# Kernel tuning notes

Hardware: AMD Instinct MI355X
Metric: run time of the kernel (lower is better)

The kernel has to match this reference:

```python
import jax, jax.numpy as jnp
import numpy as np

B, L, D, DEPTH, FF, VOCAB = 2, 2048, 1024, 4, 4096, 32000

def setup_inputs():
    key = jax.random.key(0)
    ks = jax.random.split(key, 16)
    n = lambda k, s, sc: jax.random.normal(k, s, dtype=jnp.float32) * sc
    sw = 0.01 / float(np.sqrt(D))  # xavier_normal with gain 0.01 on square dims
    return dict(
        tokens=jax.random.randint(ks[0], (B, L), 0, VOCAB),
        emb=n(ks[1], (VOCAB, D), 0.02),
        Wz=n(ks[2], (DEPTH, D, D), sw), bz=jnp.zeros((DEPTH, D)),
        Wza=n(ks[3], (DEPTH, D, D), sw), bza=jnp.zeros((DEPTH, D)),
        Wy=n(ks[4], (DEPTH, D, D), sw), by=jnp.zeros((DEPTH, D)),
        Wya=n(ks[5], (DEPTH, D, D), sw), bya=jnp.zeros((DEPTH, D)),
        lc_re=n(ks[6], (DEPTH, D), 1.0), lc_im=n(ks[7], (DEPTH, D), 1.0),
        g_in=jnp.ones((DEPTH, D)), g_sc=jnp.ones((DEPTH, D)), g_ffn=jnp.ones((DEPTH, D)),
        Wf=n(ks[8], (DEPTH, D, FF), 0.02), bf=jnp.zeros((DEPTH, FF)),
        Wfa=n(ks[9], (DEPTH, D, FF), 0.02), bfa=jnp.zeros((DEPTH, FF)),
        Wfo=n(ks[10], (DEPTH, FF, D), 0.02), bfo=jnp.zeros((DEPTH, D)),
        ln_w=jnp.ones((D,)), ln_b=jnp.zeros((D,)),
        Wout=n(ks[11], (D, VOCAB), 0.02), bout=jnp.zeros((VOCAB,)),
    )

def _silu(x):
    return x * jax.nn.sigmoid(x)

def _rms(x, w, eps=1e-6):
    return x * jax.lax.rsqrt(jnp.mean(x * x, axis=-1, keepdims=True) + eps) * w

def reference(tokens, emb, Wz, bz, Wza, bza, Wy, by, Wya, bya, lc_re, lc_im,
              g_in, g_sc, g_ffn, Wf, bf, Wfa, bfa, Wfo, bfo, ln_w, ln_b, Wout, bout):
    Bq, Lq = tokens.shape
    # Embedding with max_norm=1: torch renorms accessed rows to norm <= 1
    e = emb[tokens]
    nrm = jnp.linalg.norm(e, axis=-1, keepdims=True)
    x = e * jnp.minimum(1.0, 1.0 / jnp.maximum(nrm, 1e-7))
    # Decaying phazor kernel (shared across layers; phazor_angle_scale is a fixed buffer)
    angle = jnp.power(0.001, jnp.linspace(0.0, 1.0, D))
    ln_ph = (1e-5 + 1j * angle).astype(jnp.complex64)      # [D]
    t = jnp.arange(Lq, dtype=jnp.float32)
    ph = jnp.exp(t[:, None] * ln_ph[None, :])              # [L, D] complex
    pf = jnp.fft.fft(ph, n=2 * Lq, axis=0)                 # [2L, D]
    decay = jnp.exp(ln_ph)                                 # [D]
    for i in range(DEPTH):
        # --- SConv sublayer (pre-RMSNorm + residual) ---
        xr = x
        xn = _rms(x, g_sc[i])
        z = (xn @ Wz[i] + bz[i]) * _silu(xn @ Wza[i] + bza[i])
        zf = jnp.fft.fft(z.astype(jnp.complex64), n=2 * Lq, axis=1)
        h = jnp.fft.ifft(zf * pf[None], axis=1)[:, :Lq]    # inner-chunk causal decaying conv
        lc = (lc_re[i] + 1j * lc_im[i]).astype(jnp.complex64)
        h = h + lc[None, None, :] * ph[None] * decay[None, None, :]  # cross-chunk state carry
        y = (_rms(h.real, g_in[i]) @ Wy[i] + by[i]) * _silu(xn @ Wya[i] + bya[i])
        x = xr + y
        # --- FFN SwiGLU sublayer (pre-RMSNorm + residual) ---
        xr = x
        xn = _rms(x, g_ffn[i])
        x = xr + ((xn @ Wf[i] + bf[i]) * _silu(xn @ Wfa[i] + bfa[i])) @ Wfo[i] + bfo[i]
    # Final LayerNorm + vocab projection
    mu = jnp.mean(x, axis=-1, keepdims=True)
    var = jnp.mean((x - mu) ** 2, axis=-1, keepdims=True)
    x = (x - mu) * jax.lax.rsqrt(var + 1e-5) * ln_w + ln_b
    return x @ Wout + bout
```

## Files before the change

### kernel.cpp

```cpp
#include <hip/hip_runtime.h>
#include <math.h>

typedef __attribute__((ext_vector_type(8))) short bf16x8;
typedef __attribute__((ext_vector_type(4))) float f32x4;

#define DEVI __device__ __forceinline__

DEVI short f2bf(float f) {
  unsigned u = __builtin_bit_cast(unsigned, f);
  return (short)((u + 0x7fffu + ((u >> 16) & 1u)) >> 16);
}
DEVI float bf2f(short s) {
  unsigned u = ((unsigned)(unsigned short)s) << 16;
  return __builtin_bit_cast(float, u);
}

DEVI float silu_f(float v) { return v / (1.0f + expf(-v)); }

DEVI void async16(const void* g, void* l) {
  __builtin_amdgcn_global_load_lds(
      (const __attribute__((address_space(1))) void*)g,
      (__attribute__((address_space(3))) void*)l, 16, 0, 0);
}

template <int N>
DEVI void waitvm() { asm volatile("s_waitcnt vmcnt(%0)" ::"i"(N) : "memory"); }
DEVI void barrier_mem() { asm volatile("s_barrier" ::: "memory"); }

template <int NROWT>
DEVI void tile_map(int* bx, int* by) {
  const int nwg = gridDim.x;
  const int lin = blockIdx.x;
  const int q = nwg >> 3;
  const int wgid = (lin & 7) * q + (lin >> 3);
  *by = wgid % NROWT;
  *bx = wgid / NROWT;
}


template <int MODE, int BM, int BN, int WM, int WN, int NBUF, bool NT>
__global__ __launch_bounds__(256, 2) void gemm_k(const short* __restrict__ A,
                                                 const short* __restrict__ BT,
                                                 const float* __restrict__ bias,
                                                 void* __restrict__ outp,
                                                 int N, int K) {
  constexpr int MF = WM / 16, NF = WN / 16;
  constexpr int NWN = BN / WN;
  constexpr int PBB = (BM + BN) * 64;
  constexpr int DEPTH = NBUF - 1;
  constexpr int L = (BM + BN) / 64;
  static_assert((BM / WM) * (BN / WN) == 4, "4 waves");
  __shared__ __align__(16) char lds[NBUF * PBB];
  int bx, by;
  tile_map<4096 / BM>(&bx, &by);
  const int row0 = by * BM, col0 = bx * BN;
  const int t = threadIdx.x, w = t >> 6, lane = t & 63;
  const int wr = w / NWN, wc = w % NWN;
  f32x4 acc[MF][NF] = {};

  const int srow = t >> 2;
  const int sslot = (t & 3) ^ ((t >> 3) & 3);
  const char* gA0 = (const char*)A + ((size_t)(row0 + srow) * K) * 2 + sslot * 16;
  const char* gB0 = (const char*)BT + ((size_t)(col0 + srow) * K) * 2 + sslot * 16;
  const size_t ccstep = (size_t)K * 128;
  const int wb = w << 10;
  const int lr = lane & 15, ks = lane >> 4;

  const int NIT = K >> 5;
  auto stage = [&](int buf, int it) {
    char* dst = lds + buf * PBB;
    const size_t io = (size_t)it * 64;
#pragma unroll
    for (int cc = 0; cc < BM / 64; ++cc)
      async16(gA0 + io + cc * ccstep, dst + cc * 4096 + wb);
#pragma unroll
    for (int cc = 0; cc < BN / 64; ++cc)
      async16(gB0 + io + cc * ccstep, dst + BM * 64 + cc * 4096 + wb);
  };

#pragma unroll
  for (int pit = 0; pit < DEPTH; ++pit) stage(pit, pit);

  for (int it = 0; it < NIT; ++it) {
    const int rem = NIT - it;
    if (rem >= DEPTH + 1) waitvm<L * (DEPTH - 1)>();
    else if (rem >= 2) waitvm<L>();
    else waitvm<0>();
    barrier_mem();
    if (it + DEPTH < NIT) stage((it + DEPTH) % NBUF, it + DEPTH);
    const char* base = lds + (it % NBUF) * PBB;
    bf16x8 af[MF], bfr[NF];
#pragma unroll
    for (int m = 0; m < MF; ++m) {
      const int r = wr * WM + m * 16 + lr;
      af[m] = *(const bf16x8*)(base + r * 64 + ((ks ^ ((r >> 1) & 3)) << 4));
    }
#pragma unroll
    for (int n = 0; n < NF; ++n) {
      const int r = wc * WN + n * 16 + lr;
      bfr[n] = *(const bf16x8*)(base + BM * 64 + r * 64 + ((ks ^ ((r >> 1) & 3)) << 4));
    }
#pragma unroll
    for (int m = 0; m < MF; ++m)
#pragma unroll
      for (int n = 0; n < NF; ++n)
        acc[m][n] = __builtin_amdgcn_mfma_f32_16x16x32_bf16(af[m], bfr[n], acc[m][n], 0, 0, 0);
    __builtin_amdgcn_sched_barrier(0);
  }

  const int orow = row0 + wr * WM + (ks << 2);
  const int ocol = col0 + wc * WN + lr;
#pragma unroll
  for (int m = 0; m < MF; ++m) {
#pragma unroll
    for (int n = 0; n < NF; ++n) {
      const int c = ocol + (n << 4);
      const float bv = bias[c];
#pragma unroll
      for (int i = 0; i < 4; ++i) {
        const int r = orow + (m << 4) + i;
        const size_t idx = (size_t)r * N + c;
        float v = acc[m][n][i] + bv;
        if (MODE == 0) {
          if (NT) __builtin_nontemporal_store(v, &((float*)outp)[idx]);
          else ((float*)outp)[idx] = v;
        } else {
          ((float*)outp)[idx] += v;
        }
      }
    }
  }
}

template <int MODE, int BM, int BN, int WM, int WN, int NBUF>
__global__ __launch_bounds__(256, 2) void gemm2_k(const short* __restrict__ A1,
                                                  const short* __restrict__ A2,
                                                  const short* __restrict__ BT1,
                                                  const short* __restrict__ BT2,
                                                  const float* __restrict__ bias1,
                                                  const float* __restrict__ bias2,
                                                  void* __restrict__ outp,
                                                  int N, int K) {
  constexpr bool DUALA = (MODE == 1);
  constexpr int MF = WM / 16, NF = WN / 16;
  constexpr int NWN = BN / WN;
  constexpr int ABYTES = BM * 64 * (DUALA ? 2 : 1);
  constexpr int PBB = ABYTES + 2 * BN * 64;
  constexpr int DEPTH = NBUF - 1;
  constexpr int L = ((DUALA ? 2 : 1) * BM + 2 * BN) / 64;
  static_assert((BM / WM) * (BN / WN) == 4, "4 waves");
  __shared__ __align__(16) char lds[NBUF * PBB];
  int bx, by;
  tile_map<4096 / BM>(&bx, &by);
  const int row0 = by * BM, col0 = bx * BN;
  const int t = threadIdx.x, w = t >> 6, lane = t & 63;
  const int wr = w / NWN, wc = w % NWN;
  f32x4 acc1[MF][NF] = {}, acc2[MF][NF] = {};

  const int srow = t >> 2;
  const int sslot = (t & 3) ^ ((t >> 3) & 3);
  const size_t arow = ((size_t)(row0 + srow) * K) * 2 + sslot * 16;
  const size_t brow = ((size_t)(col0 + srow) * K) * 2 + sslot * 16;
  const char* gA1 = (const char*)A1 + arow;
  const char* gA2 = (const char*)A2 + arow;
  const char* gB1 = (const char*)BT1 + brow;
  const char* gB2 = (const char*)BT2 + brow;
  const size_t ccstep = (size_t)K * 128;
  const int wb = w << 10;
  const int lr = lane & 15, ks = lane >> 4;

  const int NIT = K >> 5;
  auto stage = [&](int buf, int it) {
    char* dst = lds + buf * PBB;
    const size_t io = (size_t)it * 64;
#pragma unroll
    for (int cc = 0; cc < BM / 64; ++cc) {
      async16(gA1 + io + cc * ccstep, dst + cc * 4096 + wb);
      if constexpr (DUALA)
        async16(gA2 + io + cc * ccstep, dst + BM * 64 + cc * 4096 + wb);
    }
#pragma unroll
    for (int cc = 0; cc < BN / 64; ++cc) {
      async16(gB1 + io + cc * ccstep, dst + ABYTES + cc * 4096 + wb);
      async16(gB2 + io + cc * ccstep, dst + ABYTES + BN * 64 + cc * 4096 + wb);
    }
  };

#pragma unroll
  for (int pit = 0; pit < DEPTH; ++pit) stage(pit, pit);

  for (int it = 0; it < NIT; ++it) {
    const int rem = NIT - it;
    if (rem >= DEPTH + 1) waitvm<L * (DEPTH - 1)>();
    else if (rem >= 2) waitvm<L>();
    else waitvm<0>();
    barrier_mem();
    if (it + DEPTH < NIT) stage((it + DEPTH) % NBUF, it + DEPTH);
    const char* base = lds + (it % NBUF) * PBB;
    bf16x8 af1[MF], af2[MF], bf1[NF], bf2[NF];
#pragma unroll
    for (int m = 0; m < MF; ++m) {
      const int r = wr * WM + m * 16 + lr;
      const int off = r * 64 + ((ks ^ ((r >> 1) & 3)) << 4);
      af1[m] = *(const bf16x8*)(base + off);
      if constexpr (DUALA) af2[m] = *(const bf16x8*)(base + BM * 64 + off);
    }
#pragma unroll
    for (int n = 0; n < NF; ++n) {
      const int r = wc * WN + n * 16 + lr;
      const int off = r * 64 + ((ks ^ ((r >> 1) & 3)) << 4);
      bf1[n] = *(const bf16x8*)(base + ABYTES + off);
      bf2[n] = *(const bf16x8*)(base + ABYTES + BN * 64 + off);
    }
#pragma unroll
    for (int m = 0; m < MF; ++m)
#pragma unroll
      for (int n = 0; n < NF; ++n) {
        acc1[m][n] = __builtin_amdgcn_mfma_f32_16x16x32_bf16(af1[m], bf1[n], acc1[m][n], 0, 0, 0);
        acc2[m][n] = __builtin_amdgcn_mfma_f32_16x16x32_bf16(DUALA ? af2[m] : af1[m], bf2[n],
                                                             acc2[m][n], 0, 0, 0);
      }
    __builtin_amdgcn_sched_barrier(0);
  }

  const int orow = row0 + wr * WM + (ks << 2);
  const int ocol = col0 + wc * WN + lr;
#pragma unroll
  for (int m = 0; m < MF; ++m) {
#pragma unroll
    for (int n = 0; n < NF; ++n) {
      const int c = ocol + (n << 4);
      const float bv1 = bias1[c], bv2 = bias2[c];
#pragma unroll
      for (int i = 0; i < 4; ++i) {
        const int r = orow + (m << 4) + i;
        const size_t idx = (size_t)r * N + c;
        const float g = (acc1[m][n][i] + bv1) * silu_f(acc2[m][n][i] + bv2);
        if (MODE == 1) ((float*)outp)[idx] += g;
        else ((short*)outp)[idx] = f2bf(g);
      }
    }
  }
}

__global__ __launch_bounds__(256) void transp_k(const float* __restrict__ W,
                                                short* __restrict__ WT,
                                                int R, int C) {
  __shared__ float tile[32][33];
  const size_t moff = (size_t)blockIdx.z * R * C;
  const float* Wp = W + moff;
  short* Tp = WT + moff;
  const int c0 = blockIdx.x << 5, r0 = blockIdx.y << 5;
  const int tx = threadIdx.x, ty = threadIdx.y;
#pragma unroll
  for (int i = 0; i < 4; ++i)
    tile[ty + 8 * i][tx] = Wp[(size_t)(r0 + ty + 8 * i) * C + (c0 + tx)];
  __syncthreads();
#pragma unroll
  for (int i = 0; i < 4; ++i)
    Tp[(size_t)(c0 + ty + 8 * i) * R + (r0 + tx)] = f2bf(tile[tx][ty + 8 * i]);
}

__global__ __launch_bounds__(256) void embed_k(const int* __restrict__ tok,
                                               const float* __restrict__ emb,
                                               float* __restrict__ x) {
  const int row = blockIdx.x, t = threadIdx.x, w = t >> 6, lane = t & 63;
  const int token = tok[row];
  float4 v = ((const float4*)(emb + (size_t)token * 1024))[t];
  float ss = v.x * v.x + v.y * v.y + v.z * v.z + v.w * v.w;
#pragma unroll
  for (int off = 32; off; off >>= 1) ss += __shfl_xor(ss, off, 64);
  __shared__ float red[4];
  if (lane == 0) red[w] = ss;
  __syncthreads();
  const float nrm = sqrtf(red[0] + red[1] + red[2] + red[3]);
  const float sc = fminf(1.0f, 1.0f / fmaxf(nrm, 1e-7f));
  v.x *= sc; v.y *= sc; v.z *= sc; v.w *= sc;
  ((float4*)(x + (size_t)row * 1024))[t] = v;
}

template <int BF>
__global__ __launch_bounds__(256) void rms_k(const void* __restrict__ xin,
                                             const float* __restrict__ g,
                                             short* __restrict__ o) {
  const int row = blockIdx.x, t = threadIdx.x, w = t >> 6, lane = t & 63;
  float v0, v1, v2, v3;
  if (BF) {
    short4 s = ((const short4*)((const short*)xin + (size_t)row * 1024))[t];
    v0 = bf2f(s.x); v1 = bf2f(s.y); v2 = bf2f(s.z); v3 = bf2f(s.w);
  } else {
    float4 v = ((const float4*)((const float*)xin + (size_t)row * 1024))[t];
    v0 = v.x; v1 = v.y; v2 = v.z; v3 = v.w;
  }
  float ss = v0 * v0 + v1 * v1 + v2 * v2 + v3 * v3;
#pragma unroll
  for (int off = 32; off; off >>= 1) ss += __shfl_xor(ss, off, 64);
  __shared__ float red[4];
  if (lane == 0) red[w] = ss;
  __syncthreads();
  const float sc = rsqrtf((red[0] + red[1] + red[2] + red[3]) * (1.0f / 1024.0f) + 1e-6f);
  float4 gv = ((const float4*)g)[t];
  short4 ov = make_short4(f2bf(v0 * sc * gv.x), f2bf(v1 * sc * gv.y),
                          f2bf(v2 * sc * gv.z), f2bf(v3 * sc * gv.w));
  *(short4*)(o + (size_t)row * 1024 + 4 * t) = ov;
}

__global__ __launch_bounds__(256) void ln_k(const float* __restrict__ x,
                                            const float* __restrict__ lw,
                                            const float* __restrict__ lb,
                                            short* __restrict__ o) {
  const int row = blockIdx.x, t = threadIdx.x, w = t >> 6, lane = t & 63;
  float4 v = ((const float4*)(x + (size_t)row * 1024))[t];
  float s1 = v.x + v.y + v.z + v.w;
  float s2 = v.x * v.x + v.y * v.y + v.z * v.z + v.w * v.w;
#pragma unroll
  for (int off = 32; off; off >>= 1) {
    s1 += __shfl_xor(s1, off, 64);
    s2 += __shfl_xor(s2, off, 64);
  }
  __shared__ float red[8];
  if (lane == 0) { red[w] = s1; red[4 + w] = s2; }
  __syncthreads();
  const float mu = (red[0] + red[1] + red[2] + red[3]) * (1.0f / 1024.0f);
  const float ex2 = (red[4] + red[5] + red[6] + red[7]) * (1.0f / 1024.0f);
  const float rs = rsqrtf(ex2 - mu * mu + 1e-5f);
  float4 wv = ((const float4*)lw)[t];
  float4 bv = ((const float4*)lb)[t];
  short4 ov = make_short4(f2bf((v.x - mu) * rs * wv.x + bv.x),
                          f2bf((v.y - mu) * rs * wv.y + bv.y),
                          f2bf((v.z - mu) * rs * wv.z + bv.z),
                          f2bf((v.w - mu) * rs * wv.w + bv.w));
  *(short4*)(o + (size_t)row * 1024 + 4 * t) = ov;
}

DEVI void decay_of(int d, float* dr, float* di) {
  const float ang = powf(1e-3f, (float)d * (1.0f / 1023.0f));
  float sn, cs;
  sincosf(ang, &sn, &cs);
  const float mag = expf(1e-5f);
  *dr = mag * cs; *di = mag * sn;
}

__global__ __launch_bounds__(256) void s1_k(const short* __restrict__ z,
                                            float* __restrict__ Er, float* __restrict__ Ei) {
  const int d = (blockIdx.x << 8) + threadIdx.x;
  const int c = blockIdx.y, b = blockIdx.z;
  float dr, di;
  decay_of(d, &dr, &di);
  const short* zp = z + ((size_t)(b * 2048 + c * 64) << 10) + d;
  float sr = 0.0f, si = 0.0f;
  for (int k = 0; k < 64; ++k) {
    float zv = bf2f(zp[(size_t)k << 10]);
    float nr = dr * sr - di * si + zv;
    si = dr * si + di * sr;
    sr = nr;
  }
  const int idx = ((b << 5) + c) * 1024 + d;
  Er[idx] = sr; Ei[idx] = si;
}

__global__ __launch_bounds__(256) void s2_k(const float* __restrict__ Er,
                                            const float* __restrict__ Ei,
                                            float* __restrict__ Sr, float* __restrict__ Si) {
  const int gid = (blockIdx.x << 8) + threadIdx.x;
  const int b = gid >> 10, d = gid & 1023;
  float dr, di;
  decay_of(d, &dr, &di);
  float ar = dr, ai = di;
#pragma unroll
  for (int q = 0; q < 6; ++q) { float nr = ar * ar - ai * ai; ai = 2.0f * ar * ai; ar = nr; }
  float sr = 0.0f, si = 0.0f;
  for (int c = 0; c < 32; ++c) {
    const int idx = ((b << 5) + c) * 1024 + d;
    Sr[idx] = sr; Si[idx] = si;
    const float er = Er[idx], ei = Ei[idx];
    const float nr = ar * sr - ai * si + er;
    si = ar * si + ai * sr + ei;
    sr = nr;
  }
}

__global__ __launch_bounds__(256) void s3_k(const short* __restrict__ z,
                                            const float* __restrict__ Sr,
                                            const float* __restrict__ Si,
                                            const float* __restrict__ lcre,
                                            const float* __restrict__ lcim,
                                            short* __restrict__ h) {
  const int d = (blockIdx.x << 8) + threadIdx.x;
  const int c = blockIdx.y, b = blockIdx.z;
  float dr, di;
  decay_of(d, &dr, &di);
  float ar = dr, ai = di;
#pragma unroll
  for (int q = 0; q < 6; ++q) { float nr = ar * ar - ai * ai; ai = 2.0f * ar * ai; ar = nr; }
  float wr = 1.0f, wi = 0.0f, br = ar, bi = ai;
  int e = c;
  while (e) {
    if (e & 1) { float nr = wr * br - wi * bi; wi = wr * bi + wi * br; wr = nr; }
    float nb = br * br - bi * bi; bi = 2.0f * br * bi; br = nb;
    e >>= 1;
  }
  { float nr = wr * dr - wi * di; wi = wr * di + wi * dr; wr = nr; }
  const int idx = ((b << 5) + c) * 1024 + d;
  float sr = Sr[idx], si = Si[idx];
  const float lr_ = lcre[d], li_ = lcim[d];
  const size_t base = ((size_t)(b * 2048 + c * 64) << 10) + d;
  for (int k = 0; k < 64; ++k) {
    const float zv = bf2f(z[base + ((size_t)k << 10)]);
    const float nr = dr * sr - di * si + zv;
    si = dr * si + di * sr;
    sr = nr;
    h[base + ((size_t)k << 10)] = f2bf(sr + lr_ * wr - li_ * wi);
    const float nw = wr * dr - wi * di;
    wi = wr * di + wi * dr;
    wr = nw;
  }
}

extern "C" void kernel_launch(void* const* d_in, const int* in_sizes, int n_in,
                              void* d_out, int out_size, void* d_ws, size_t ws_size,
                              hipStream_t stream) {
  const int* tokens = (const int*)d_in[0];
  const float* emb = (const float*)d_in[1];
  const float* Wz = (const float*)d_in[2];
  const float* bz = (const float*)d_in[3];
  const float* Wza = (const float*)d_in[4];
  const float* bza = (const float*)d_in[5];
  const float* Wy = (const float*)d_in[6];
  const float* by = (const float*)d_in[7];
  const float* Wya = (const float*)d_in[8];
  const float* bya = (const float*)d_in[9];
  const float* lc_re = (const float*)d_in[10];
  const float* lc_im = (const float*)d_in[11];
  const float* g_in = (const float*)d_in[12];
  const float* g_sc = (const float*)d_in[13];
  const float* g_ffn = (const float*)d_in[14];
  const float* Wf = (const float*)d_in[15];
  const float* bf = (const float*)d_in[16];
  const float* Wfa = (const float*)d_in[17];
  const float* bfa = (const float*)d_in[18];
  const float* Wfo = (const float*)d_in[19];
  const float* bfo = (const float*)d_in[20];
  const float* ln_w = (const float*)d_in[21];
  const float* ln_b = (const float*)d_in[22];
  const float* Wout = (const float*)d_in[23];
  const float* bout = (const float*)d_in[24];

  char* p = (char*)d_ws;
  float* xb = (float*)p;   p += (size_t)4096 * 1024 * 4;
  short* zb = (short*)p;   p += (size_t)4096 * 1024 * 2;
  short* hb = (short*)p;   p += (size_t)4096 * 1024 * 2;
  float* Er = (float*)p;   p += (size_t)2 * 32 * 1024 * 4;
  float* Ei = (float*)p;   p += (size_t)2 * 32 * 1024 * 4;
  float* Sr = (float*)p;   p += (size_t)2 * 32 * 1024 * 4;
  float* Si = (float*)p;   p += (size_t)2 * 32 * 1024 * 4;
  short* xnb = (short*)p;  p += (size_t)4096 * 1024 * 2;
  short* hnb = (short*)p;  p += (size_t)4096 * 1024 * 2;
  short* gb = (short*)p;   p += (size_t)4096 * 4096 * 2;
  short* WzT = (short*)p;  p += (size_t)4 * 1024 * 1024 * 2;
  short* WzaT = (short*)p; p += (size_t)4 * 1024 * 1024 * 2;
  short* WyT = (short*)p;  p += (size_t)4 * 1024 * 1024 * 2;
  short* WyaT = (short*)p; p += (size_t)4 * 1024 * 1024 * 2;
  short* WfT = (short*)p;  p += (size_t)4 * 1024 * 4096 * 2;
  short* WfaT = (short*)p; p += (size_t)4 * 1024 * 4096 * 2;
  short* WfoT = (short*)p; p += (size_t)4 * 1024 * 4096 * 2;
  short* WoutT = (short*)p; p += (size_t)32000 * 1024 * 2;

  const dim3 tb(32, 8);
  transp_k<<<dim3(32, 32, 4), tb, 0, stream>>>(Wz, WzT, 1024, 1024);
  transp_k<<<dim3(32, 32, 4), tb, 0, stream>>>(Wza, WzaT, 1024, 1024);
  transp_k<<<dim3(32, 32, 4), tb, 0, stream>>>(Wy, WyT, 1024, 1024);
  transp_k<<<dim3(32, 32, 4), tb, 0, stream>>>(Wya, WyaT, 1024, 1024);
  transp_k<<<dim3(128, 32, 4), tb, 0, stream>>>(Wf, WfT, 1024, 4096);
  transp_k<<<dim3(128, 32, 4), tb, 0, stream>>>(Wfa, WfaT, 1024, 4096);
  transp_k<<<dim3(32, 128, 4), tb, 0, stream>>>(Wfo, WfoT, 4096, 1024);
  transp_k<<<dim3(1000, 32, 1), tb, 0, stream>>>(Wout, WoutT, 1024, 32000);

  embed_k<<<4096, 256, 0, stream>>>(tokens, emb, xb);

  for (int i = 0; i < 4; ++i) {
    const size_t dd = (size_t)i * 1024 * 1024;
    const size_t dv = (size_t)i * 1024;
    const size_t dw = (size_t)i * 1024 * 4096;
    const size_t df = (size_t)i * 4096;
    rms_k<0><<<4096, 256, 0, stream>>>(xb, g_sc + dv, xnb);
    gemm2_k<2, 128, 128, 64, 64, 3><<<256, 256, 0, stream>>>(
        xnb, xnb, WzT + dd, WzaT + dd, bz + dv, bza + dv, zb, 1024, 1024);
    s1_k<<<dim3(4, 32, 2), 256, 0, stream>>>(zb, Er, Ei);
    s2_k<<<8, 256, 0, stream>>>(Er, Ei, Sr, Si);
    s3_k<<<dim3(4, 32, 2), 256, 0, stream>>>(zb, Sr, Si, lc_re + dv, lc_im + dv, hb);
    rms_k<1><<<4096, 256, 0, stream>>>(hb, g_in + dv, hnb);
    gemm2_k<1, 64, 128, 32, 64, 3><<<512, 256, 0, stream>>>(
        hnb, xnb, WyT + dd, WyaT + dd, by + dv, bya + dv, xb, 1024, 1024);
    rms_k<0><<<4096, 256, 0, stream>>>(xb, g_ffn + dv, xnb);
    gemm2_k<2, 128, 128, 64, 64, 3><<<1024, 256, 0, stream>>>(
        xnb, xnb, WfT + dw, WfaT + dw, bf + df, bfa + df, gb, 4096, 1024);
    gemm_k<4, 128, 128, 64, 64, 3, false><<<256, 256, 0, stream>>>(
        gb, WfoT + dw, bfo + dv, xb, 1024, 4096);
  }

  ln_k<<<4096, 256, 0, stream>>>(xb, ln_w, ln_b, xnb);
  gemm_k<0, 128, 256, 128, 64, 3, true><<<4000, 256, 0, stream>>>(
      xnb, WoutT, bout, (float*)d_out, 32000, 1024);

  (void)in_sizes; (void)n_in; (void)out_size; (void)ws_size;
}
```

Baseline: 1.642 ms.

## Add 8-wave 256x256 GEMM kernels for vocab projection and FFN gate

Adds two new 512-thread GEMM kernels with double-buffered LDS staging, split K-half loads that overlap MFMA work, and s_setprio around the MFMA blocks. gemm8_k uses a 256x256 output tile for the 32000-wide vocab projection. dual8_k computes the SwiGLU FFN up projection with a 256x128 tile, sharing one A tile across both weight matrices. The larger tiles are meant to cut global and LDS traffic per FLOP and to hide load latency behind compute, at the cost of higher register and LDS pressure per block. The nontemporal store option on the output GEMM is also removed.

```diff
diff --git a/kernel.cpp b/kernel.cpp
--- a/kernel.cpp
+++ b/kernel.cpp
@@ -26,6 +26,10 @@
 template <int N>
 DEVI void waitvm() { asm volatile("s_waitcnt vmcnt(%0)" ::"i"(N) : "memory"); }
 DEVI void barrier_mem() { asm volatile("s_barrier" ::: "memory"); }
+DEVI void lgkm0_sb() {
+  asm volatile("s_waitcnt lgkmcnt(0)" ::: "memory");
+  __builtin_amdgcn_sched_barrier(0);
+}
 
 template <int NROWT>
 DEVI void tile_map(int* bx, int* by) {
@@ -37,8 +41,221 @@
   *bx = wgid / NROWT;
 }
 
-
-template <int MODE, int BM, int BN, int WM, int WN, int NBUF, bool NT>
+#define SWZ(r) ((ks ^ (((r) >> 1) & 3)) << 4)
+
+__global__ __launch_bounds__(512, 2) void gemm8_k(const short* __restrict__ A,
+                                                  const short* __restrict__ BT,
+                                                  const float* __restrict__ bias,
+                                                  float* __restrict__ outp,
+                                                  int N, int K) {
+  __shared__ __align__(16) char lds[2 * 65536];
+  int bx, by;
+  tile_map<16>(&bx, &by);
+  const int row0 = by << 8, col0 = bx << 8;
+  const int t = threadIdx.x, w = t >> 6, lane = t & 63;
+  const int wm = w >> 2, wn = w & 3;
+  const int lr = lane & 15, ks = lane >> 4;
+  f32x4 acc[8][4] = {};
+
+  const int sslot = (t & 3) ^ ((t >> 3) & 3);
+  const char* gA = (const char*)A + ((size_t)(row0 + (t >> 2)) * K) * 2 + sslot * 16;
+  const char* gB = (const char*)BT + ((size_t)(col0 + (t >> 2)) * K) * 2 + sslot * 16;
+  const size_t cstep = (size_t)K << 8;
+  const int t16 = t << 4;
+
+  const int nkt = K >> 6;
+
+#define SA8(nb, kt, s)                                                        \
+  {                                                                           \
+    const size_t co = (size_t)(kt) * 128 + (s) * 64;                          \
+    async16(gA + co, (nb) + (s) * 16384 + t16);                               \
+    async16(gA + cstep + co, (nb) + (s) * 16384 + 8192 + t16);                \
+  }
+#define SB8(nb, kt, s)                                                        \
+  {                                                                           \
+    const size_t co = (size_t)(kt) * 128 + (s) * 64;                          \
+    async16(gB + co, (nb) + 32768 + (s) * 16384 + t16);                       \
+    async16(gB + cstep + co, (nb) + 32768 + (s) * 16384 + 8192 + t16);        \
+  }
+#define RB8(s)                                                                \
+  _Pragma("unroll") for (int n = 0; n < 4; ++n) {                             \
+    const int rb = (wn << 6) + (n << 4) + lr;                                 \
+    bfr[n] = *(const bf16x8*)(base + 32768 + (s) * 16384 + rb * 64 + SWZ(rb)); \
+  }
+#define RA8(s, mh)                                                            \
+  _Pragma("unroll") for (int m = 0; m < 4; ++m) {                             \
+    const int r = (wm << 7) + (mh) * 64 + (m << 4) + lr;                      \
+    af[m] = *(const bf16x8*)(base + (s) * 16384 + r * 64 + SWZ(r));           \
+  }
+#define MM8(mh)                                                               \
+  __builtin_amdgcn_s_setprio(1);                                              \
+  _Pragma("unroll") for (int m = 0; m < 4; ++m)                               \
+  _Pragma("unroll") for (int n = 0; n < 4; ++n)                               \
+      acc[(mh) * 4 + m][n] = __builtin_amdgcn_mfma_f32_16x16x32_bf16(         \
+          af[m], bfr[n], acc[(mh) * 4 + m][n], 0, 0, 0);                      \
+  __builtin_amdgcn_s_setprio(0);                                              \
+  __builtin_amdgcn_sched_barrier(0);
+
+  {
+    char* nb = lds;
+    SA8(nb, 0, 0); SB8(nb, 0, 0); SA8(nb, 0, 1); SB8(nb, 0, 1);
+  }
+
+  for (int kt = 0; kt < nkt; ++kt) {
+    const int ktn = kt + 1;
+    const char* base = lds + (kt & 1) * 65536;
+    char* nb = lds + (ktn & 1) * 65536;
+    bf16x8 af[4], bfr[4];
+    waitvm<4>();
+    barrier_mem();
+    if (ktn < nkt) SA8(nb, ktn, 0);
+    RB8(0); RA8(0, 0);
+    lgkm0_sb();
+    MM8(0);
+    barrier_mem();
+    if (ktn < nkt) SB8(nb, ktn, 0);
+    RA8(0, 1);
+    lgkm0_sb();
+    MM8(1);
+    if (ktn < nkt) waitvm<4>();
+    else waitvm<0>();
+    barrier_mem();
+    if (ktn < nkt) SA8(nb, ktn, 1);
+    RB8(1); RA8(1, 0);
+    lgkm0_sb();
+    MM8(0);
+    barrier_mem();
+    if (ktn < nkt) SB8(nb, ktn, 1);
+    RA8(1, 1);
+    lgkm0_sb();
+    MM8(1);
+  }
+
+  const int orow = row0 + (wm << 7) + (ks << 2);
+  const int ocol = col0 + (wn << 6) + lr;
+#pragma unroll
+  for (int mf = 0; mf < 8; ++mf) {
+#pragma unroll
+    for (int n = 0; n < 4; ++n) {
+      const int c = ocol + (n << 4);
+      const float bv = bias[c];
+#pragma unroll
+      for (int i = 0; i < 4; ++i) {
+        const int r = orow + (mf << 4) + i;
+        outp[(size_t)r * N + c] = acc[mf][n][i] + bv;
+      }
+    }
+  }
+#undef SA8
+#undef SB8
+#undef RB8
+#undef RA8
+#undef MM8
+}
+
+__global__ __launch_bounds__(512, 2) void dual8_k(const short* __restrict__ A,
+                                                  const short* __restrict__ BT1,
+                                                  const short* __restrict__ BT2,
+                                                  const float* __restrict__ bias1,
+                                                  const float* __restrict__ bias2,
+                                                  short* __restrict__ outp,
+                                                  int N, int K) {
+  __shared__ __align__(16) char lds[2 * 32768];
+  int bx, by;
+  tile_map<16>(&bx, &by);
+  const int row0 = by << 8, col0 = bx << 7;
+  const int t = threadIdx.x, w = t >> 6, lane = t & 63;
+  const int wm = w >> 1, wn = w & 1;
+  const int lr = lane & 15, ks = lane >> 4;
+  f32x4 acc1[4][4] = {}, acc2[4][4] = {};
+
+  const int sslot = (t & 3) ^ ((t >> 3) & 3);
+  const char* gA = (const char*)A + ((size_t)(row0 + (t >> 2)) * K) * 2 + sslot * 16;
+  const char* gB1 = (const char*)BT1 + ((size_t)(col0 + (t >> 2)) * K) * 2 + sslot * 16;
+  const char* gB2 = (const char*)BT2 + ((size_t)(col0 + (t >> 2)) * K) * 2 + sslot * 16;
+  const size_t cstep = (size_t)K << 8;
+  const int t16 = t << 4;
+  const int nkt = K >> 5;
+
+#define SAD(nb, kt)                                                           \
+  {                                                                           \
+    const size_t co = (size_t)(kt) * 64;                                      \
+    async16(gA + co, (nb) + t16);                                             \
+    async16(gA + cstep + co, (nb) + 8192 + t16);                              \
+  }
+#define SB1D(nb, kt) async16(gB1 + (size_t)(kt) * 64, (nb) + 16384 + t16)
+#define SB2D(nb, kt) async16(gB2 + (size_t)(kt) * 64, (nb) + 24576 + t16)
+
+  { char* nb = lds; SAD(nb, 0); SB1D(nb, 0); SB2D(nb, 0); }
+
+  for (int kt = 0; kt < nkt; ++kt) {
+    const int ktn = kt + 1;
+    const char* base = lds + (kt & 1) * 32768;
+    char* nb = lds + (ktn & 1) * 32768;
+    bf16x8 af[4], bfr[4];
+    waitvm<1>();
+    barrier_mem();
+    if (ktn < nkt) { SAD(nb, ktn); SB1D(nb, ktn); }
+#pragma unroll
+    for (int n = 0; n < 4; ++n) {
+      const int rb = (wn << 6) + (n << 4) + lr;
+      bfr[n] = *(const bf16x8*)(base + 16384 + rb * 64 + SWZ(rb));
+    }
+#pragma unroll
+    for (int m = 0; m < 4; ++m) {
+      const int r = (wm << 6) + (m << 4) + lr;
+      af[m] = *(const bf16x8*)(base + r * 64 + SWZ(r));
+    }
+    lgkm0_sb();
+    __builtin_amdgcn_s_setprio(1);
+#pragma unroll
+    for (int m = 0; m < 4; ++m)
+#pragma unroll
+      for (int n = 0; n < 4; ++n)
+        acc1[m][n] = __builtin_amdgcn_mfma_f32_16x16x32_bf16(af[m], bfr[n], acc1[m][n], 0, 0, 0);
+    __builtin_amdgcn_s_setprio(0);
+    __builtin_amdgcn_sched_barrier(0);
+    if (ktn < nkt) waitvm<3>();
+    else waitvm<0>();
+    barrier_mem();
+    if (ktn < nkt) SB2D(nb, ktn);
+#pragma unroll
+    for (int n = 0; n < 4; ++n) {
+      const int rb = (wn << 6) + (n << 4) + lr;
+      bfr[n] = *(const bf16x8*)(base + 24576 + rb * 64 + SWZ(rb));
+    }
+    lgkm0_sb();
+    __builtin_amdgcn_s_setprio(1);
+#pragma unroll
+    for (int m = 0; m < 4; ++m)
+#pragma unroll
+      for (int n = 0; n < 4; ++n)
+        acc2[m][n] = __builtin_amdgcn_mfma_f32_16x16x32_bf16(af[m], bfr[n], acc2[m][n], 0, 0, 0);
+    __builtin_amdgcn_s_setprio(0);
+    __builtin_amdgcn_sched_barrier(0);
+  }
+
+  const int orow = row0 + (wm << 6) + (ks << 2);
+  const int ocol = col0 + (wn << 6) + lr;
+#pragma unroll
+  for (int m = 0; m < 4; ++m) {
+#pragma unroll
+    for (int n = 0; n < 4; ++n) {
+      const int c = ocol + (n << 4);
+      const float bv1 = bias1[c], bv2 = bias2[c];
+#pragma unroll
+      for (int i = 0; i < 4; ++i) {
+        const int r = orow + (m << 4) + i;
+        outp[(size_t)r * N + c] = f2bf((acc1[m][n][i] + bv1) * silu_f(acc2[m][n][i] + bv2));
+      }
+    }
+  }
+#undef SAD
+#undef SB1D
+#undef SB2D
+}
+
+template <int MODE, int BM, int BN, int WM, int WN, int NBUF>
 __global__ __launch_bounds__(256, 2) void gemm_k(const short* __restrict__ A,
                                                  const short* __restrict__ BT,
                                                  const float* __restrict__ bias,
@@ -58,10 +275,9 @@
   const int wr = w / NWN, wc = w % NWN;
   f32x4 acc[MF][NF] = {};
 
-  const int srow = t >> 2;
   const int sslot = (t & 3) ^ ((t >> 3) & 3);
-  const char* gA0 = (const char*)A + ((size_t)(row0 + srow) * K) * 2 + sslot * 16;
-  const char* gB0 = (const char*)BT + ((size_t)(col0 + srow) * K) * 2 + sslot * 16;
+  const char* gA0 = (const char*)A + ((size_t)(row0 + (t >> 2)) * K) * 2 + sslot * 16;
+  const char* gB0 = (const char*)BT + ((size_t)(col0 + (t >> 2)) * K) * 2 + sslot * 16;
   const size_t ccstep = (size_t)K * 128;
   const int wb = w << 10;
   const int lr = lane & 15, ks = lane >> 4;
@@ -93,12 +309,12 @@
 #pragma unroll
     for (int m = 0; m < MF; ++m) {
       const int r = wr * WM + m * 16 + lr;
-      af[m] = *(const bf16x8*)(base + r * 64 + ((ks ^ ((r >> 1) & 3)) << 4));
+      af[m] = *(const bf16x8*)(base + r * 64 + SWZ(r));
     }
 #pragma unroll
     for (int n = 0; n < NF; ++n) {
       const int r = wc * WN + n * 16 + lr;
-      bfr[n] = *(const bf16x8*)(base + BM * 64 + r * 64 + ((ks ^ ((r >> 1) & 3)) << 4));
+      bfr[n] = *(const bf16x8*)(base + BM * 64 + r * 64 + SWZ(r));
     }
 #pragma unroll
     for (int m = 0; m < MF; ++m)
@@ -121,12 +337,8 @@
         const int r = orow + (m << 4) + i;
         const size_t idx = (size_t)r * N + c;
         float v = acc[m][n][i] + bv;
-        if (MODE == 0) {
-          if (NT) __builtin_nontemporal_store(v, &((float*)outp)[idx]);
-          else ((float*)outp)[idx] = v;
-        } else {
-          ((float*)outp)[idx] += v;
-        }
+        if (MODE == 0) ((float*)outp)[idx] = v;
+        else ((float*)outp)[idx] += v;
       }
     }
   }
@@ -157,10 +369,9 @@
   const int wr = w / NWN, wc = w % NWN;
   f32x4 acc1[MF][NF] = {}, acc2[MF][NF] = {};
 
-  const int srow = t >> 2;
   const int sslot = (t & 3) ^ ((t >> 3) & 3);
-  const size_t arow = ((size_t)(row0 + srow) * K) * 2 + sslot * 16;
-  const size_t brow = ((size_t)(col0 + srow) * K) * 2 + sslot * 16;
+  const size_t arow = ((size_t)(row0 + (t >> 2)) * K) * 2 + sslot * 16;
+  const size_t brow = ((size_t)(col0 + (t >> 2)) * K) * 2 + sslot * 16;
   const char* gA1 = (const char*)A1 + arow;
   const char* gA2 = (const char*)A2 + arow;
   const char* gB1 = (const char*)BT1 + brow;
@@ -201,14 +412,14 @@
 #pragma unroll
     for (int m = 0; m < MF; ++m) {
       const int r = wr * WM + m * 16 + lr;
-      const int off = r * 64 + ((ks ^ ((r >> 1) & 3)) << 4);
+      const int off = r * 64 + SWZ(r);
       af1[m] = *(const bf16x8*)(base + off);
       if constexpr (DUALA) af2[m] = *(const bf16x8*)(base + BM * 64 + off);
     }
 #pragma unroll
     for (int n = 0; n < NF; ++n) {
       const int r = wc * WN + n * 16 + lr;
-      const int off = r * 64 + ((ks ^ ((r >> 1) & 3)) << 4);
+      const int off = r * 64 + SWZ(r);
       bf1[n] = *(const bf16x8*)(base + ABYTES + off);
       bf2[n] = *(const bf16x8*)(base + ABYTES + BN * 64 + off);
     }
@@ -493,15 +704,14 @@
     gemm2_k<1, 64, 128, 32, 64, 3><<<512, 256, 0, stream>>>(
         hnb, xnb, WyT + dd, WyaT + dd, by + dv, bya + dv, xb, 1024, 1024);
     rms_k<0><<<4096, 256, 0, stream>>>(xb, g_ffn + dv, xnb);
-    gemm2_k<2, 128, 128, 64, 64, 3><<<1024, 256, 0, stream>>>(
-        xnb, xnb, WfT + dw, WfaT + dw, bf + df, bfa + df, gb, 4096, 1024);
-    gemm_k<4, 128, 128, 64, 64, 3, false><<<256, 256, 0, stream>>>(
+    dual8_k<<<512, 512, 0, stream>>>(xnb, WfT + dw, WfaT + dw, bf + df, bfa + df,
+                                     gb, 4096, 1024);
+    gemm_k<4, 128, 128, 64, 64, 3><<<256, 256, 0, stream>>>(
         gb, WfoT + dw, bfo + dv, xb, 1024, 4096);
   }
 
   ln_k<<<4096, 256, 0, stream>>>(xb, ln_w, ln_b, xnb);
-  gemm_k<0, 128, 256, 128, 64, 3, true><<<4000, 256, 0, stream>>>(
-      xnb, WoutT, bout, (float*)d_out, 32000, 1024);
+  gemm8_k<<<2000, 512, 0, stream>>>(xnb, WoutT, bout, (float*)d_out, 32000, 1024);
 
   (void)in_sizes; (void)n_in; (void)out_size; (void)ws_size;
 }
```

New measurement: 1.598 ms. -2.7%, faster.
